# Optimization experiments

Measured on AMD Instinct MI355X. Metric: run time of the kernel, lower is better.

Reference implementation:

```python
import jax, jax.numpy as jnp
import numpy as np

TOPK = 4

def setup_inputs() -> dict:
    key = jax.random.key(0)
    k1, k2, k3 = jax.random.split(key, 3)
    B, K, C, L = 8, 8, 256, 4096
    xs = jax.random.normal(k1, (B, K, C, L), dtype=jnp.float32)
    # scores are assumed softmax-normalized routing scores in the original
    logits = jax.random.normal(k2, (B, K), dtype=jnp.float32)
    scores = jax.nn.softmax(logits, axis=-1)
    expert_w = jax.random.normal(k3, (K, C, C), dtype=jnp.float32) * 0.02
    expert_b = jnp.zeros((K, C), dtype=jnp.float32)
    return {"xs": xs, "scores": scores, "expert_w": expert_w, "expert_b": expert_b}

def reference(xs, scores, expert_w, expert_b):
    B, K, C, L = xs.shape
    # HardTopKRouting: hard top-k selection, weights renormalized.
    # Backward of the routing is STE returning zero grad to scores.
    tw, sel = jax.lax.top_k(jax.lax.stop_gradient(scores), TOPK)  # [B, topk]
    tw = tw / (tw.sum(axis=-1, keepdims=True) + 1e-8)
    # Dense per-(sample, expert) combine weight; zero for unselected experts.
    w_full = jnp.zeros((B, K), dtype=xs.dtype).at[
        jnp.arange(B)[:, None], sel
    ].set(tw)  # [B, K]
    # Per-expert module (stand-in for Mamba): channel-mixing linear on C.
    # y[b,k,d,l] = sum_c expert_w[k,d,c] * xs[b,k,c,l] + expert_b[k,d]
    y = jnp.einsum('bkcl,kdc->bkdl', xs, expert_w) + expert_b[None, :, :, None]
    # Weighted scatter-add combine: unselected experts have weight 0,
    # matching the original's sparse dispatch/combine math exactly.
    out = jnp.einsum('bk,bkdl->bdl', w_full, y)  # [B, C, L]
    return out
```

## Files before the change

kernel.cpp:

```cpp
#include <hip/hip_runtime.h>

#define B_ 8
#define K_ 8
#define C_ 256
#define L_ 4096
#define TOPK_ 4
#define BN 64
#define BK 32
#define LDST 40

typedef __attribute__((ext_vector_type(8))) short bf16x8;
typedef __attribute__((ext_vector_type(4))) float f32x4;

union P8 { bf16x8 v; unsigned short s[8]; };
union F4 { float4 v; float f[4]; };

__device__ __forceinline__ unsigned short f2bf(float x) {
  unsigned u = __float_as_uint(x);
  u += 0x7fffu + ((u >> 16) & 1u);
  return (unsigned short)(u >> 16);
}

__global__ void route_kernel(const float* __restrict__ scores,
                             float* __restrict__ wts,
                             int* __restrict__ sel) {
  int b = threadIdx.x;
  if (b < B_) {
    float s[K_];
#pragma unroll
    for (int k = 0; k < K_; ++k) s[k] = scores[b * K_ + k];
    float tw[TOPK_]; int ch[TOPK_];
    float sum = 0.f;
#pragma unroll
    for (int i = 0; i < TOPK_; ++i) {
      float bv = -1e30f; int bk = 0;
#pragma unroll
      for (int k = 0; k < K_; ++k) {
        if (s[k] > bv) { bv = s[k]; bk = k; }
      }
      ch[i] = bk; tw[i] = bv; sum += bv;
      s[bk] = -1e30f;
    }
    float inv = 1.f / (sum + 1e-8f);
#pragma unroll
    for (int i = 0; i < TOPK_; ++i) {
      wts[b * TOPK_ + i] = tw[i] * inv;
      sel[b * TOPK_ + i] = ch[i];
    }
  }
}

__global__ __launch_bounds__(256, 2)
void moe_main(const float* __restrict__ xs, const float* __restrict__ ew,
              const float* __restrict__ eb, const float* __restrict__ wts,
              const int* __restrict__ sel, float* __restrict__ out) {
  __shared__ alignas(16) unsigned short As[C_ * LDST];
  __shared__ alignas(16) unsigned short Bs[BN * LDST];
  __shared__ float biasc[C_];

  const int t = threadIdx.x;
  const int b = blockIdx.y;
  const int l0 = blockIdx.x * BN;
  const int wave = t >> 6;
  const int lane = t & 63;
  const int l16 = lane & 15;
  const int quad = lane >> 4;
  const int cb = (t >> 4) * 8;
  const int loff = (t & 15) * 4;

  float w_s[TOPK_]; int k_s[TOPK_];
#pragma unroll
  for (int i = 0; i < TOPK_; ++i) {
    w_s[i] = wts[b * TOPK_ + i];
    k_s[i] = sel[b * TOPK_ + i];
  }

  {
    float a = 0.f;
#pragma unroll
    for (int i = 0; i < TOPK_; ++i) a += w_s[i] * eb[k_s[i] * C_ + t];
    biasc[t] = a;
  }

  f32x4 acc[4][4];
#pragma unroll
  for (int mi = 0; mi < 4; ++mi)
#pragma unroll
    for (int ni = 0; ni < 4; ++ni)
      acc[mi][ni] = (f32x4){0.f, 0.f, 0.f, 0.f};

  F4 ar[8], br[8];

  auto issue_loads = [&](int slot, int c0) {
    const float* ewk = ew + (size_t)k_s[slot] * C_ * C_ + (size_t)t * C_ + c0;
#pragma unroll
    for (int j = 0; j < 8; ++j) ar[j].v = ((const float4*)ewk)[j];
    if (t < 64) {
      const float* xp = xs + (((size_t)b * K_ + k_s[slot]) * C_ + (size_t)(c0 + cb)) * L_ + l0 + loff;
#pragma unroll
      for (int j = 0; j < 8; ++j) br[j].v = *(const float4*)(xp + (size_t)j * L_);
    }
  };

  issue_loads(0, 0);

  for (int step = 0; step < 32; ++step) {
    __syncthreads();
    {
      unsigned short* arow = As + t * LDST;
#pragma unroll
      for (int g = 0; g < 4; ++g) {
        P8 p;
#pragma unroll
        for (int e = 0; e < 4; ++e) {
          p.s[e]     = f2bf(ar[2 * g].f[e]);
          p.s[4 + e] = f2bf(ar[2 * g + 1].f[e]);
        }
        *(bf16x8*)(arow + g * 8) = p.v;
      }
      if (t < 64) {
        float w = w_s[step >> 3];
#pragma unroll
        for (int i = 0; i < 4; ++i) {
          P8 p;
#pragma unroll
          for (int j = 0; j < 8; ++j) p.s[j] = f2bf(w * br[j].f[i]);
          *(bf16x8*)(Bs + (size_t)(loff + i) * LDST + cb) = p.v;
        }
      }
    }
    __syncthreads();
    if (step + 1 < 32) issue_loads((step + 1) >> 3, ((step + 1) & 7) * BK);

    bf16x8 af[4], bfr[4];
#pragma unroll
    for (int mi = 0; mi < 4; ++mi)
      af[mi] = *(const bf16x8*)(As + (size_t)(wave * 64 + mi * 16 + l16) * LDST + quad * 8);
#pragma unroll
    for (int ni = 0; ni < 4; ++ni)
      bfr[ni] = *(const bf16x8*)(Bs + (size_t)(ni * 16 + l16) * LDST + quad * 8);
#pragma unroll
    for (int mi = 0; mi < 4; ++mi)
#pragma unroll
      for (int ni = 0; ni < 4; ++ni)
        acc[mi][ni] = __builtin_amdgcn_mfma_f32_16x16x32_bf16(af[mi], bfr[ni], acc[mi][ni], 0, 0, 0);
  }

#pragma unroll
  for (int mi = 0; mi < 4; ++mi) {
#pragma unroll
    for (int r = 0; r < 4; ++r) {
      int d = wave * 64 + mi * 16 + quad * 4 + r;
      float bias = biasc[d];
#pragma unroll
      for (int ni = 0; ni < 4; ++ni) {
        out[((size_t)b * C_ + d) * L_ + l0 + ni * 16 + l16] = acc[mi][ni][r] + bias;
      }
    }
  }
}

extern "C" void kernel_launch(void* const* d_in, const int* in_sizes, int n_in,
                              void* d_out, int out_size, void* d_ws, size_t ws_size,
                              hipStream_t stream) {
  const float* xs     = (const float*)d_in[0];
  const float* scores = (const float*)d_in[1];
  const float* ew     = (const float*)d_in[2];
  const float* eb     = (const float*)d_in[3];
  float* out = (float*)d_out;

  float* wts = (float*)d_ws;
  int*   sel = (int*)((char*)d_ws + 256);

  route_kernel<<<1, 64, 0, stream>>>(scores, wts, sel);
  dim3 grid(L_ / BN, B_);
  moe_main<<<grid, 256, 0, stream>>>(xs, ew, eb, wts, sel, out);
}
```

Before: 413.6 us.

## Prepack routing-scaled bf16 expert weights and double-buffer wider L tiles

A prep kernel now runs the routing once per (sample, slot), folds each routing weight into a bf16 copy of the selected expert weights laid out for tile loading, and precomputes the combined bias. The main GEMM loads this prepacked bf16 weight directly instead of converting fp32 per block. It uses 128-wide L tiles so each weight tile is reused across more columns, spreads xs loads across all threads, and double-buffers shared memory to drop one barrier per step. In exchange it adds an extra kernel that writes about 4 MB of weight copies, and the larger tile and accumulator set lowers occupancy to one block per SM.

```diff
diff --git a/kernel.cpp b/kernel.cpp
--- a/kernel.cpp
+++ b/kernel.cpp
@@ -5,7 +5,7 @@
 #define C_ 256
 #define L_ 4096
 #define TOPK_ 4
-#define BN 64
+#define BN 128
 #define BK 32
 #define LDST 40
 
@@ -21,42 +21,65 @@
   return (unsigned short)(u >> 16);
 }
 
-__global__ void route_kernel(const float* __restrict__ scores,
-                             float* __restrict__ wts,
-                             int* __restrict__ sel) {
-  int b = threadIdx.x;
-  if (b < B_) {
-    float s[K_];
+__device__ __forceinline__ void route_b(const float* __restrict__ scores, int b,
+                                        float w[TOPK_], int kk[TOPK_]) {
+  float s[K_];
 #pragma unroll
-    for (int k = 0; k < K_; ++k) s[k] = scores[b * K_ + k];
-    float tw[TOPK_]; int ch[TOPK_];
-    float sum = 0.f;
+  for (int k = 0; k < K_; ++k) s[k] = scores[b * K_ + k];
+  float sum = 0.f;
 #pragma unroll
-    for (int i = 0; i < TOPK_; ++i) {
-      float bv = -1e30f; int bk = 0;
+  for (int i = 0; i < TOPK_; ++i) {
+    float bv = -1e30f; int bk = 0;
 #pragma unroll
-      for (int k = 0; k < K_; ++k) {
-        if (s[k] > bv) { bv = s[k]; bk = k; }
-      }
-      ch[i] = bk; tw[i] = bv; sum += bv;
-      s[bk] = -1e30f;
-    }
-    float inv = 1.f / (sum + 1e-8f);
+    for (int k = 0; k < K_; ++k)
+      if (s[k] > bv) { bv = s[k]; bk = k; }
+    kk[i] = bk; w[i] = bv; sum += bv;
+    s[bk] = -1e30f;
+  }
+  float inv = 1.f / (sum + 1e-8f);
 #pragma unroll
-    for (int i = 0; i < TOPK_; ++i) {
-      wts[b * TOPK_ + i] = tw[i] * inv;
-      sel[b * TOPK_ + i] = ch[i];
-    }
+  for (int i = 0; i < TOPK_; ++i) w[i] *= inv;
+}
+
+__global__ __launch_bounds__(256)
+void prep_kernel(const float* __restrict__ scores, const float* __restrict__ ew,
+                 const float* __restrict__ eb, int* __restrict__ sel,
+                 float* __restrict__ biasc, unsigned short* __restrict__ ewb) {
+  const int blk = blockIdx.x;
+  const int b = blk >> 2, i = blk & 3;
+  const int t = threadIdx.x;
+  float w[TOPK_]; int kk[TOPK_];
+  route_b(scores, b, w, kk);
+  if (i == 0) {
+    if (t < TOPK_) sel[b * TOPK_ + t] = kk[t];
+    float a = 0.f;
+#pragma unroll
+    for (int j = 0; j < TOPK_; ++j) a += w[j] * eb[kk[j] * C_ + t];
+    biasc[b * C_ + t] = a;
+  }
+  const float wi = w[i];
+  const float* src = ew + (size_t)kk[i] * C_ * C_;
+  unsigned short* dst = ewb + (size_t)blk * (C_ * C_);
+  for (int j = 0; j < 32; ++j) {
+    int m = t + 256 * j;
+    int d = (m >> 2) & 255;
+    int cb = m >> 10;
+    int ci = (m & 3) * 8;
+    const float* sp = src + d * C_ + cb * 32 + ci;
+    F4 a0, a1; a0.v = *(const float4*)sp; a1.v = *(const float4*)(sp + 4);
+    P8 p;
+#pragma unroll
+    for (int e = 0; e < 4; ++e) { p.s[e] = f2bf(wi * a0.f[e]); p.s[4 + e] = f2bf(wi * a1.f[e]); }
+    *(bf16x8*)(dst + (size_t)m * 8) = p.v;
   }
 }
 
-__global__ __launch_bounds__(256, 2)
-void moe_main(const float* __restrict__ xs, const float* __restrict__ ew,
-              const float* __restrict__ eb, const float* __restrict__ wts,
-              const int* __restrict__ sel, float* __restrict__ out) {
-  __shared__ alignas(16) unsigned short As[C_ * LDST];
-  __shared__ alignas(16) unsigned short Bs[BN * LDST];
-  __shared__ float biasc[C_];
+__global__ __launch_bounds__(256, 1)
+void moe_main(const float* __restrict__ xs, const unsigned short* __restrict__ ewb,
+              const float* __restrict__ biasc, const int* __restrict__ sel,
+              float* __restrict__ out) {
+  __shared__ alignas(16) unsigned short As[2][C_ * LDST];
+  __shared__ alignas(16) unsigned short Bs[2][BN * LDST];
 
   const int t = threadIdx.x;
   const int b = blockIdx.y;
@@ -65,97 +88,76 @@
   const int lane = t & 63;
   const int l16 = lane & 15;
   const int quad = lane >> 4;
-  const int cb = (t >> 4) * 8;
-  const int loff = (t & 15) * 4;
+  const int lq = (t & 31) * 4;
+  const int cq = (t >> 5) * 4;
 
-  float w_s[TOPK_]; int k_s[TOPK_];
+  int k_s[TOPK_];
 #pragma unroll
-  for (int i = 0; i < TOPK_; ++i) {
-    w_s[i] = wts[b * TOPK_ + i];
-    k_s[i] = sel[b * TOPK_ + i];
-  }
+  for (int i = 0; i < TOPK_; ++i) k_s[i] = sel[b * TOPK_ + i];
 
-  {
-    float a = 0.f;
-#pragma unroll
-    for (int i = 0; i < TOPK_; ++i) a += w_s[i] * eb[k_s[i] * C_ + t];
-    biasc[t] = a;
-  }
-
-  f32x4 acc[4][4];
+  f32x4 acc[4][8];
 #pragma unroll
   for (int mi = 0; mi < 4; ++mi)
 #pragma unroll
-    for (int ni = 0; ni < 4; ++ni)
+    for (int ni = 0; ni < 8; ++ni)
       acc[mi][ni] = (f32x4){0.f, 0.f, 0.f, 0.f};
 
-  F4 ar[8], br[8];
+  const unsigned short* ewb_b = ewb + (size_t)b * TOPK_ * (C_ * C_);
 
-  auto issue_loads = [&](int slot, int c0) {
-    const float* ewk = ew + (size_t)k_s[slot] * C_ * C_ + (size_t)t * C_ + c0;
+  bf16x8 ar[4]; F4 br[4];
+  auto issue = [&](int s) {
+    const int slot = s >> 3, cb = s & 7;
+    const unsigned short* ap = ewb_b + (size_t)slot * (C_ * C_) + cb * 8192 + t * 32;
 #pragma unroll
-    for (int j = 0; j < 8; ++j) ar[j].v = ((const float4*)ewk)[j];
-    if (t < 64) {
-      const float* xp = xs + (((size_t)b * K_ + k_s[slot]) * C_ + (size_t)(c0 + cb)) * L_ + l0 + loff;
+    for (int j = 0; j < 4; ++j) ar[j] = *(const bf16x8*)(ap + j * 8);
+    const float* xp = xs + (((size_t)b * K_ + k_s[slot]) * C_ + (size_t)(cb * 32 + cq)) * L_ + l0 + lq;
 #pragma unroll
-      for (int j = 0; j < 8; ++j) br[j].v = *(const float4*)(xp + (size_t)j * L_);
-    }
+    for (int j = 0; j < 4; ++j) br[j].v = *(const float4*)(xp + (size_t)j * L_);
   };
 
-  issue_loads(0, 0);
-
-  for (int step = 0; step < 32; ++step) {
-    __syncthreads();
+  issue(0);
+  for (int s = 0; s < 32; ++s) {
+    const int buf = s & 1;
     {
-      unsigned short* arow = As + t * LDST;
+      unsigned short* arow = As[buf] + t * LDST;
 #pragma unroll
-      for (int g = 0; g < 4; ++g) {
-        P8 p;
+      for (int j = 0; j < 4; ++j) *(bf16x8*)(arow + j * 8) = ar[j];
 #pragma unroll
-        for (int e = 0; e < 4; ++e) {
-          p.s[e]     = f2bf(ar[2 * g].f[e]);
-          p.s[4 + e] = f2bf(ar[2 * g + 1].f[e]);
-        }
-        *(bf16x8*)(arow + g * 8) = p.v;
-      }
-      if (t < 64) {
-        float w = w_s[step >> 3];
+      for (int i2 = 0; i2 < 4; ++i2) {
+        union { unsigned short s4[4]; unsigned long long u; } p;
 #pragma unroll
-        for (int i = 0; i < 4; ++i) {
-          P8 p;
-#pragma unroll
-          for (int j = 0; j < 8; ++j) p.s[j] = f2bf(w * br[j].f[i]);
-          *(bf16x8*)(Bs + (size_t)(loff + i) * LDST + cb) = p.v;
-        }
+        for (int j = 0; j < 4; ++j) p.s4[j] = f2bf(br[j].f[i2]);
+        *(unsigned long long*)(Bs[buf] + (size_t)(lq + i2) * LDST + cq) = p.u;
       }
     }
+    if (s + 1 < 32) issue(s + 1);
     __syncthreads();
-    if (step + 1 < 32) issue_loads((step + 1) >> 3, ((step + 1) & 7) * BK);
 
-    bf16x8 af[4], bfr[4];
+    bf16x8 af[4], bfr[8];
 #pragma unroll
     for (int mi = 0; mi < 4; ++mi)
-      af[mi] = *(const bf16x8*)(As + (size_t)(wave * 64 + mi * 16 + l16) * LDST + quad * 8);
+      af[mi] = *(const bf16x8*)(As[buf] + (size_t)(wave * 64 + mi * 16 + l16) * LDST + quad * 8);
 #pragma unroll
-    for (int ni = 0; ni < 4; ++ni)
-      bfr[ni] = *(const bf16x8*)(Bs + (size_t)(ni * 16 + l16) * LDST + quad * 8);
+    for (int ni = 0; ni < 8; ++ni)
+      bfr[ni] = *(const bf16x8*)(Bs[buf] + (size_t)(ni * 16 + l16) * LDST + quad * 8);
 #pragma unroll
     for (int mi = 0; mi < 4; ++mi)
 #pragma unroll
-      for (int ni = 0; ni < 4; ++ni)
+      for (int ni = 0; ni < 8; ++ni)
         acc[mi][ni] = __builtin_amdgcn_mfma_f32_16x16x32_bf16(af[mi], bfr[ni], acc[mi][ni], 0, 0, 0);
   }
 
+  const float* bc = biasc + b * C_;
 #pragma unroll
   for (int mi = 0; mi < 4; ++mi) {
 #pragma unroll
     for (int r = 0; r < 4; ++r) {
-      int d = wave * 64 + mi * 16 + quad * 4 + r;
-      float bias = biasc[d];
+      const int d = wave * 64 + mi * 16 + quad * 4 + r;
+      const float bias = bc[d];
+      float* orow = out + ((size_t)b * C_ + d) * L_ + l0;
 #pragma unroll
-      for (int ni = 0; ni < 4; ++ni) {
-        out[((size_t)b * C_ + d) * L_ + l0 + ni * 16 + l16] = acc[mi][ni][r] + bias;
-      }
+      for (int ni = 0; ni < 8; ++ni)
+        orow[ni * 16 + l16] = acc[mi][ni][r] + bias;
     }
   }
 }
@@ -169,10 +171,11 @@
   const float* eb     = (const float*)d_in[3];
   float* out = (float*)d_out;
 
-  float* wts = (float*)d_ws;
-  int*   sel = (int*)((char*)d_ws + 256);
+  int*   sel   = (int*)d_ws;
+  float* biasc = (float*)((char*)d_ws + 1024);
+  unsigned short* ewb = (unsigned short*)((char*)d_ws + 16384);
 
-  route_kernel<<<1, 64, 0, stream>>>(scores, wts, sel);
+  prep_kernel<<<B_ * TOPK_, 256, 0, stream>>>(scores, ew, eb, sel, biasc, ewb);
   dim3 grid(L_ / BN, B_);
-  moe_main<<<grid, 256, 0, stream>>>(xs, ew, eb, wts, sel, out);
+  moe_main<<<grid, 256, 0, stream>>>(xs, ewb, biasc, sel, out);
 }
```

Result: faster. 348.5 us (-15.7%).
